# Kernel tuning notes

Measured on AMD Instinct MI355X. Metric: run time of the kernel, lower is better.

The kernel has to match this reference:

```python
import jax, jax.numpy as jnp
import numpy as np

COMMITMENT_COST = 0.25


def setup_inputs() -> dict:
    key = jax.random.key(0)
    k1, k2 = jax.random.split(key)
    n_embeddings, embedding_dim = 1024, 256
    x = jax.random.normal(k1, (32, 2048, embedding_dim), dtype=jnp.float32)
    r = 1.0 / n_embeddings
    embedding = jax.random.uniform(k2, (n_embeddings, embedding_dim),
                                   dtype=jnp.float32, minval=-r, maxval=r)
    return {"x": x, "embedding": embedding}


def reference(x, embedding):
    M, D = embedding.shape
    # x is detached before flattening in the original quantize()
    x_flat = jax.lax.stop_gradient(x).reshape(-1, D)  # [N, D]
    distances = (jnp.sum(embedding * embedding, axis=1)
                 + jnp.sum(x_flat * x_flat, axis=1, keepdims=True)
                 - 2.0 * (x_flat @ embedding.T))  # [N, M]
    indices = jnp.argmin(distances, axis=-1)  # [N] int
    quantized = embedding[indices].reshape(x.shape)  # gather + view_as(x)
    # commitment loss: quantized is detached in the loss term
    e_latent_loss = jnp.mean(jnp.square(x - jax.lax.stop_gradient(quantized)))
    loss = COMMITMENT_COST * e_latent_loss
    return quantized, loss, indices
```

## Files before the change

kernel.cpp:

```cpp
#include <hip/hip_runtime.h>

#define N_ROWS   65536
#define D        256
#define D4       64
#define M        1024
#define LOSS_OFF 16777216
#define IDX_OFF  16777217
#define COMMIT_SCALE (0.25f / 16777216.0f)
#define E_SCALE  1024.0f
#define C_SCALE  0.001953125f

typedef _Float16 f16x8 __attribute__((ext_vector_type(8)));
typedef _Float16 f16x4 __attribute__((ext_vector_type(4)));
typedef float    f32x4 __attribute__((ext_vector_type(4)));

__device__ __forceinline__ float np_block128(const float* __restrict__ a, int l) {
    float r0 = __fmul_rn(a[l +   0], a[l +   0]);
    float r1 = __fmul_rn(a[l +  16], a[l +  16]);
    float r2 = __fmul_rn(a[l +  32], a[l +  32]);
    float r3 = __fmul_rn(a[l +  48], a[l +  48]);
    float r4 = __fmul_rn(a[l +  64], a[l +  64]);
    float r5 = __fmul_rn(a[l +  80], a[l +  80]);
    float r6 = __fmul_rn(a[l +  96], a[l +  96]);
    float r7 = __fmul_rn(a[l + 112], a[l + 112]);
    return __fadd_rn(__fadd_rn(__fadd_rn(r0, r1), __fadd_rn(r2, r3)),
                     __fadd_rn(__fadd_rn(r4, r5), __fadd_rn(r6, r7)));
}
__device__ __forceinline__ float np_reduce16(float v) {
    float s = __fadd_rn(v, __shfl_down(v, 8));
    s = __fadd_rn(s, __shfl_down(s, 4));
    s = __fadd_rn(s, __shfl_down(s, 2));
    s = __fadd_rn(s, __shfl_down(s, 1));
    return s;
}

__global__ __launch_bounds__(256) void norms_kernel(
    const float4* __restrict__ x4, const float4* __restrict__ emb4,
    float* __restrict__ bsq, float* __restrict__ esq,
    _Float16* __restrict__ e_hi, _Float16* __restrict__ e_mid,
    float* __restrict__ loss_slot) {
    __shared__ float rowbuf[16 * 260];
    const int tid = threadIdx.x;
    const float4* src4;
    float* dst;
    int row0;
    const bool is_emb = blockIdx.x >= 4096;
    if (!is_emb) {
        row0 = blockIdx.x * 16;
        src4 = x4 + (size_t)row0 * 64;
        dst = bsq + row0;
    } else {
        row0 = (blockIdx.x - 4096) * 16;
        src4 = emb4 + (size_t)row0 * 64;
        dst = esq + row0;
    }
    #pragma unroll
    for (int p = 0; p < 4; ++p) {
        const int f = tid + p * 256;
        const int r = f >> 6, c4 = f & 63;
        *(float4*)&rowbuf[r * 260 + c4 * 4] = src4[f];
    }
    __syncthreads();
    const int l = tid & 15, g = tid >> 4;
    const float* base = &rowbuf[g * 260];
    const float v0 = np_block128(base, l);
    const float v1 = np_block128(base + 128, l);
    const float t0 = np_reduce16(v0);
    const float t1 = np_reduce16(v1);
    if (l == 0) dst[g] = __fadd_rn(t0, t1);
    if (blockIdx.x == 0 && tid == 0) *loss_slot = 0.0f;

    if (is_emb) {
        #pragma unroll
        for (int p = 0; p < 4; ++p) {
            const int f = tid + p * 256;
            const int r = f >> 6, k4 = f & 63;
            const int code = row0 + r;
            const int kc = k4 >> 3, k8 = k4 & 7;
            const int q = k8 >> 1, half = k8 & 1;
            const int jt = code >> 7, cl = code & 127;
            const int cg = cl >> 4, lmc = cl & 15;
            float4 v = *(const float4*)&rowbuf[r * 260 + k4 * 4];
            float a[4] = {v.x * E_SCALE, v.y * E_SCALE,
                          v.z * E_SCALE, v.w * E_SCALE};
            f16x4 hi, mid;
            #pragma unroll
            for (int j = 0; j < 4; ++j) {
                _Float16 h = (_Float16)a[j];
                float rr = __fsub_rn(a[j], (float)h);
                hi[j] = h;
                mid[j] = (_Float16)rr;
            }
            const size_t ofs = (size_t)kc * 32768 + (size_t)jt * 4096
                             + (size_t)(cg * 64 + q * 16 + lmc) * 8 + half * 4;
            *(f16x4*)&e_hi[ofs]  = hi;
            *(f16x4*)&e_mid[ofs] = mid;
        }
    }
}

__global__ __launch_bounds__(256, 2) void argmin_mfma_kernel(
    const float* __restrict__ x,
    const _Float16* __restrict__ e_hi, const _Float16* __restrict__ e_mid,
    const float* __restrict__ esq, const float* __restrict__ bsq,
    float* __restrict__ idx_out_f, int* __restrict__ idx_out_i) {
    __shared__ float esq_lds[1024];
    __shared__ float red_d[64][2];
    __shared__ int   red_i[64][2];

    const int tid = threadIdx.x;
    const int w = tid >> 6, lane = tid & 63;
    const int w_row = w >> 1, w_col = w & 1;
    const int lm = lane & 15, q = lane >> 4;
    const int row0 = blockIdx.x * 64;

    f16x8 a_hi[2][8], a_mid[2][8];
    #pragma unroll
    for (int fm = 0; fm < 2; ++fm) {
        const float* xr = x + (size_t)(row0 + w_row * 32 + fm * 16 + lm) * D + q * 8;
        #pragma unroll
        for (int kc = 0; kc < 8; ++kc) {
            float4 v0 = *(const float4*)(xr + kc * 32);
            float4 v1 = *(const float4*)(xr + kc * 32 + 4);
            float e[8] = {v0.x, v0.y, v0.z, v0.w, v1.x, v1.y, v1.z, v1.w};
            #pragma unroll
            for (int j = 0; j < 8; ++j) {
                _Float16 h = (_Float16)e[j];
                float r = __fsub_rn(e[j], (float)h);
                a_hi[fm][kc][j]  = h;
                a_mid[fm][kc][j] = (_Float16)r;
            }
        }
    }
    float bq[2][4];
    #pragma unroll
    for (int fm = 0; fm < 2; ++fm)
        #pragma unroll
        for (int r = 0; r < 4; ++r)
            bq[fm][r] = bsq[row0 + w_row * 32 + fm * 16 + q * 4 + r];

    *(float4*)&esq_lds[tid * 4] = ((const float4*)esq)[tid];
    __syncthreads();

    float best[2][4] = {{3.0e38f, 3.0e38f, 3.0e38f, 3.0e38f},
                        {3.0e38f, 3.0e38f, 3.0e38f, 3.0e38f}};
    int bidx[2][4] = {{0, 0, 0, 0}, {0, 0, 0, 0}};

    const int fofs = (w_col * 4) * 512 + lane * 8;
    for (int jt = 0; jt < 8; ++jt) {
        const int j0 = jt * 128;
        f32x4 acc[2][4] = {};
        #pragma unroll
        for (int kc = 0; kc < 8; ++kc) {
            const size_t cb = (size_t)kc * 32768 + (size_t)jt * 4096 + fofs;
            f16x8 bh[4], bm[4];
            #pragma unroll
            for (int fn = 0; fn < 4; ++fn) {
                bh[fn] = *(const f16x8*)&e_hi[cb + fn * 512];
                bm[fn] = *(const f16x8*)&e_mid[cb + fn * 512];
            }
            #pragma unroll
            for (int fm = 0; fm < 2; ++fm)
                #pragma unroll
                for (int fn = 0; fn < 4; ++fn) {
                    acc[fm][fn] = __builtin_amdgcn_mfma_f32_16x16x32_f16(
                        a_hi[fm][kc], bh[fn], acc[fm][fn], 0, 0, 0);
                    acc[fm][fn] = __builtin_amdgcn_mfma_f32_16x16x32_f16(
                        a_mid[fm][kc], bh[fn], acc[fm][fn], 0, 0, 0);
                    acc[fm][fn] = __builtin_amdgcn_mfma_f32_16x16x32_f16(
                        a_hi[fm][kc], bm[fn], acc[fm][fn], 0, 0, 0);
                }
        }
        #pragma unroll
        for (int fn = 0; fn < 4; ++fn) {
            const int j = j0 + w_col * 64 + fn * 16 + lm;
            const float eq = esq_lds[j];
            #pragma unroll
            for (int fm = 0; fm < 2; ++fm)
                #pragma unroll
                for (int r = 0; r < 4; ++r) {
                    const float d = __fsub_rn(__fadd_rn(eq, bq[fm][r]),
                                              acc[fm][fn][r] * C_SCALE);
                    if (d < best[fm][r]) { best[fm][r] = d; bidx[fm][r] = j; }
                }
        }
    }
    #pragma unroll
    for (int fm = 0; fm < 2; ++fm)
        #pragma unroll
        for (int r = 0; r < 4; ++r) {
            float d = best[fm][r]; int i = bidx[fm][r];
            #pragma unroll
            for (int mv = 1; mv <= 8; mv <<= 1) {
                const float d2 = __shfl_xor(d, mv, 64);
                const int   i2 = __shfl_xor(i, mv, 64);
                if (d2 < d || (d2 == d && i2 < i)) { d = d2; i = i2; }
            }
            best[fm][r] = d; bidx[fm][r] = i;
        }
    __syncthreads();
    if (lm == 0) {
        #pragma unroll
        for (int fm = 0; fm < 2; ++fm)
            #pragma unroll
            for (int r = 0; r < 4; ++r) {
                const int rl = w_row * 32 + fm * 16 + q * 4 + r;
                red_d[rl][w_col] = best[fm][r];
                red_i[rl][w_col] = bidx[fm][r];
            }
    }
    __syncthreads();
    if (tid < 64) {
        float d0 = red_d[tid][0]; int i0 = red_i[tid][0];
        const float d1 = red_d[tid][1]; const int i1 = red_i[tid][1];
        if (d1 < d0 || (d1 == d0 && i1 < i0)) { d0 = d1; i0 = i1; }
        idx_out_f[row0 + tid] = (float)i0;
        idx_out_i[row0 + tid] = i0;
    }
}

__global__ __launch_bounds__(256) void gather_loss_kernel(
    const float4* __restrict__ x4, const float4* __restrict__ emb4,
    const int* __restrict__ idx, float4* __restrict__ q4,
    float* __restrict__ loss_slot) {
    const int base = blockIdx.x * 256 + threadIdx.x;
    float acc = 0.0f;
    #pragma unroll
    for (int i = 0; i < 16; ++i) {
        const int f   = base + i * (1024 * 256);
        const int row = f >> 6;
        const int c4  = f & 63;
        const int e   = idx[row];
        float4 qv = emb4[e * D4 + c4];
        float4 xv = x4[f];
        q4[f] = qv;
        const float dx = xv.x - qv.x, dy = xv.y - qv.y;
        const float dz = xv.z - qv.z, dw = xv.w - qv.w;
        acc += dx * dx + dy * dy + dz * dz + dw * dw;
    }
    #pragma unroll
    for (int off = 32; off; off >>= 1) acc += __shfl_down(acc, off, 64);
    __shared__ float wsum[4];
    const int lane = threadIdx.x & 63, w = threadIdx.x >> 6;
    if (lane == 0) wsum[w] = acc;
    __syncthreads();
    if (threadIdx.x == 0) {
        atomicAdd(loss_slot, (wsum[0] + wsum[1] + wsum[2] + wsum[3]) * COMMIT_SCALE);
    }
}

extern "C" void kernel_launch(void* const* d_in, const int* in_sizes, int n_in,
                              void* d_out, int out_size, void* d_ws, size_t ws_size,
                              hipStream_t stream) {
    const float* x   = (const float*)d_in[0];
    const float* emb = (const float*)d_in[1];
    float* out = (float*)d_out;
    float*    bsq  = (float*)d_ws;
    float*    esq  = bsq + N_ROWS;
    int*      idx  = (int*)(esq + M);
    _Float16* e_hi = (_Float16*)(idx + N_ROWS);
    _Float16* e_mid = e_hi + (size_t)M * D;

    norms_kernel<<<4096 + M / 16, 256, 0, stream>>>((const float4*)x,
                                                    (const float4*)emb,
                                                    bsq, esq, e_hi, e_mid,
                                                    out + LOSS_OFF);
    argmin_mfma_kernel<<<N_ROWS / 64, 256, 0, stream>>>(x, e_hi, e_mid,
                                                        esq, bsq,
                                                        out + IDX_OFF, idx);
    gather_loss_kernel<<<1024, 256, 0, stream>>>((const float4*)x,
                                                 (const float4*)emb, idx,
                                                 (float4*)out, out + LOSS_OFF);
}
```

Baseline: 267.7 us.

## Double-buffer codebook fragments via async global-to-LDS DMA per wave

Codebook hi/mid fp16 fragments were loaded directly from global memory into registers before each MFMA group. They now arrive through per-wave double-buffered LDS slots filled with global_load_lds async copies, issued two chunks ahead and guarded by vmcnt waits. Wave priority is raised around the MFMA block so math overlaps the next DMA. This aims to hide global load latency, at the cost of 64KB of extra LDS per block, which may reduce occupancy below the launch-bound target of 2 blocks.

```diff
diff --git a/kernel.cpp b/kernel.cpp
--- a/kernel.cpp
+++ b/kernel.cpp
@@ -13,6 +13,12 @@
 typedef _Float16 f16x8 __attribute__((ext_vector_type(8)));
 typedef _Float16 f16x4 __attribute__((ext_vector_type(4)));
 typedef float    f32x4 __attribute__((ext_vector_type(4)));
+
+__device__ __forceinline__ void async_copy16(const void* g, void* l) {
+    __builtin_amdgcn_global_load_lds(
+        (const __attribute__((address_space(1))) unsigned int*)g,
+        (__attribute__((address_space(3))) unsigned int*)l, 16, 0, 0);
+}
 
 __device__ __forceinline__ float np_block128(const float* __restrict__ a, int l) {
     float r0 = __fmul_rn(a[l +   0], a[l +   0]);
@@ -104,6 +110,7 @@
     const _Float16* __restrict__ e_hi, const _Float16* __restrict__ e_mid,
     const float* __restrict__ esq, const float* __restrict__ bsq,
     float* __restrict__ idx_out_f, int* __restrict__ idx_out_i) {
+    __shared__ __attribute__((aligned(16))) _Float16 buf[4][2][4096];
     __shared__ float esq_lds[1024];
     __shared__ float red_d[64][2];
     __shared__ int   red_i[64][2];
@@ -114,6 +121,26 @@
     const int lm = lane & 15, q = lane >> 4;
     const int row0 = blockIdx.x * 64;
 
+    auto dma = [&](int c, int s) {
+        const int jt = c >> 3, kc = c & 7;
+        const size_t gofs = (size_t)kc * 65536 + (size_t)jt * 8192
+                          + (size_t)w_col * 4096 + (size_t)lane * 16;
+        const char* gh = (const char*)e_hi + gofs;
+        const char* gm = (const char*)e_mid + gofs;
+        _Float16* lh  = &buf[w][s][0];
+        _Float16* lmm = &buf[w][s][2048];
+        async_copy16(gh,        lh);
+        async_copy16(gh + 1024, lh + 512);
+        async_copy16(gh + 2048, lh + 1024);
+        async_copy16(gh + 3072, lh + 1536);
+        async_copy16(gm,        lmm);
+        async_copy16(gm + 1024, lmm + 512);
+        async_copy16(gm + 2048, lmm + 1024);
+        async_copy16(gm + 3072, lmm + 1536);
+    };
+
+    dma(0, 0);
+
     f16x8 a_hi[2][8], a_mid[2][8];
     #pragma unroll
     for (int fm = 0; fm < 2; ++fm) {
@@ -140,25 +167,32 @@
             bq[fm][r] = bsq[row0 + w_row * 32 + fm * 16 + q * 4 + r];
 
     *(float4*)&esq_lds[tid * 4] = ((const float4*)esq)[tid];
-    __syncthreads();
+
+    asm volatile("s_waitcnt vmcnt(0) lgkmcnt(0)" ::: "memory");
+    __syncthreads();
+    dma(1, 1);
 
     float best[2][4] = {{3.0e38f, 3.0e38f, 3.0e38f, 3.0e38f},
                         {3.0e38f, 3.0e38f, 3.0e38f, 3.0e38f}};
     int bidx[2][4] = {{0, 0, 0, 0}, {0, 0, 0, 0}};
 
-    const int fofs = (w_col * 4) * 512 + lane * 8;
     for (int jt = 0; jt < 8; ++jt) {
         const int j0 = jt * 128;
         f32x4 acc[2][4] = {};
         #pragma unroll
         for (int kc = 0; kc < 8; ++kc) {
-            const size_t cb = (size_t)kc * 32768 + (size_t)jt * 4096 + fofs;
+            const int c = jt * 8 + kc;
+            const int P = c & 1;
             f16x8 bh[4], bm[4];
             #pragma unroll
             for (int fn = 0; fn < 4; ++fn) {
-                bh[fn] = *(const f16x8*)&e_hi[cb + fn * 512];
-                bm[fn] = *(const f16x8*)&e_mid[cb + fn * 512];
-            }
+                bh[fn] = *(const f16x8*)&buf[w][P][fn * 512 + lane * 8];
+                bm[fn] = *(const f16x8*)&buf[w][P][2048 + fn * 512 + lane * 8];
+            }
+            asm volatile("s_waitcnt lgkmcnt(0)" ::: "memory");
+            __builtin_amdgcn_sched_barrier(0);
+            if (c < 62) dma(c + 2, P);
+            __builtin_amdgcn_s_setprio(1);
             #pragma unroll
             for (int fm = 0; fm < 2; ++fm)
                 #pragma unroll
@@ -170,6 +204,12 @@
                     acc[fm][fn] = __builtin_amdgcn_mfma_f32_16x16x32_f16(
                         a_hi[fm][kc], bm[fn], acc[fm][fn], 0, 0, 0);
                 }
+            __builtin_amdgcn_s_setprio(0);
+            if (c < 62)
+                asm volatile("s_waitcnt vmcnt(8)" ::: "memory");
+            else if (c == 62)
+                asm volatile("s_waitcnt vmcnt(0)" ::: "memory");
+            __builtin_amdgcn_sched_barrier(0);
         }
         #pragma unroll
         for (int fn = 0; fn < 4; ++fn) {
```

New measurement: 244.9 us. 1.09x faster.

## Stage codebook tiles through double-buffered LDS via async global_load_lds

Applied to the files above, without the earlier changes.

Codebook hi/mid fp16 tiles were read straight from global memory into registers by every wave. They are now copied cooperatively into a double-buffered 64KB shared-memory staging area with global_load_lds, and the next group is prefetched while the current one feeds the MFMAs. Each wave loads its B fragments from LDS and raises its scheduling priority around the MFMA block. The aim is to hide global load latency and remove duplicate codebook reads across waves. The costs are a barrier per group, a larger LDS footprint that may limit occupancy to two blocks per CU, and full vmcnt waits that serialize part of the pipeline.

```diff
diff --git a/kernel.cpp b/kernel.cpp
--- a/kernel.cpp
+++ b/kernel.cpp
@@ -13,6 +13,12 @@
 typedef _Float16 f16x8 __attribute__((ext_vector_type(8)));
 typedef _Float16 f16x4 __attribute__((ext_vector_type(4)));
 typedef float    f32x4 __attribute__((ext_vector_type(4)));
+
+__device__ __forceinline__ void async_copy16(const void* g, void* l) {
+    __builtin_amdgcn_global_load_lds(
+        (const __attribute__((address_space(1))) unsigned int*)g,
+        (__attribute__((address_space(3))) unsigned int*)l, 16, 0, 0);
+}
 
 __device__ __forceinline__ float np_block128(const float* __restrict__ a, int l) {
     float r0 = __fmul_rn(a[l +   0], a[l +   0]);
@@ -104,6 +110,7 @@
     const _Float16* __restrict__ e_hi, const _Float16* __restrict__ e_mid,
     const float* __restrict__ esq, const float* __restrict__ bsq,
     float* __restrict__ idx_out_f, int* __restrict__ idx_out_i) {
+    __shared__ __attribute__((aligned(16))) _Float16 buf[2][16384];
     __shared__ float esq_lds[1024];
     __shared__ float red_d[64][2];
     __shared__ int   red_i[64][2];
@@ -114,6 +121,21 @@
     const int lm = lane & 15, q = lane >> 4;
     const int row0 = blockIdx.x * 64;
 
+    const int p_sub = w >> 1, p_plane = w & 1;
+    const _Float16* p_src = p_plane ? e_mid : e_hi;
+    auto dma_group = [&](int g, int s) {
+        const int jt = g >> 2, kc0 = (g & 3) * 2;
+        const char* gp = (const char*)p_src
+                       + (size_t)(kc0 + p_sub) * 65536 + (size_t)jt * 8192
+                       + (size_t)lane * 16;
+        _Float16* lp = &buf[s][p_sub * 8192 + p_plane * 4096];
+        #pragma unroll
+        for (int u = 0; u < 8; ++u)
+            async_copy16(gp + u * 1024, lp + u * 512);
+    };
+
+    dma_group(0, 0);
+
     f16x8 a_hi[2][8], a_mid[2][8];
     #pragma unroll
     for (int fm = 0; fm < 2; ++fm) {
@@ -140,36 +162,53 @@
             bq[fm][r] = bsq[row0 + w_row * 32 + fm * 16 + q * 4 + r];
 
     *(float4*)&esq_lds[tid * 4] = ((const float4*)esq)[tid];
+
+    asm volatile("s_waitcnt vmcnt(0) lgkmcnt(0)" ::: "memory");
     __syncthreads();
 
     float best[2][4] = {{3.0e38f, 3.0e38f, 3.0e38f, 3.0e38f},
                         {3.0e38f, 3.0e38f, 3.0e38f, 3.0e38f}};
     int bidx[2][4] = {{0, 0, 0, 0}, {0, 0, 0, 0}};
 
-    const int fofs = (w_col * 4) * 512 + lane * 8;
     for (int jt = 0; jt < 8; ++jt) {
         const int j0 = jt * 128;
         f32x4 acc[2][4] = {};
         #pragma unroll
-        for (int kc = 0; kc < 8; ++kc) {
-            const size_t cb = (size_t)kc * 32768 + (size_t)jt * 4096 + fofs;
-            f16x8 bh[4], bm[4];
-            #pragma unroll
-            for (int fn = 0; fn < 4; ++fn) {
-                bh[fn] = *(const f16x8*)&e_hi[cb + fn * 512];
-                bm[fn] = *(const f16x8*)&e_mid[cb + fn * 512];
-            }
-            #pragma unroll
-            for (int fm = 0; fm < 2; ++fm)
+        for (int gi = 0; gi < 4; ++gi) {
+            const int g = jt * 4 + gi;
+            if (g) {
+                asm volatile("s_waitcnt vmcnt(0) lgkmcnt(0)\n\t"
+                             "s_barrier" ::: "memory");
+                __builtin_amdgcn_sched_barrier(0);
+            }
+            if (g < 31) dma_group(g + 1, (g + 1) & 1);
+            const int s = g & 1;
+            #pragma unroll
+            for (int sub = 0; sub < 2; ++sub) {
+                const int kc = gi * 2 + sub;
+                f16x8 bh[4], bm[4];
+                const int fb = sub * 8192 + (w_col * 4) * 512 + lane * 8;
                 #pragma unroll
                 for (int fn = 0; fn < 4; ++fn) {
-                    acc[fm][fn] = __builtin_amdgcn_mfma_f32_16x16x32_f16(
-                        a_hi[fm][kc], bh[fn], acc[fm][fn], 0, 0, 0);
-                    acc[fm][fn] = __builtin_amdgcn_mfma_f32_16x16x32_f16(
-                        a_mid[fm][kc], bh[fn], acc[fm][fn], 0, 0, 0);
-                    acc[fm][fn] = __builtin_amdgcn_mfma_f32_16x16x32_f16(
-                        a_hi[fm][kc], bm[fn], acc[fm][fn], 0, 0, 0);
+                    bh[fn] = *(const f16x8*)&buf[s][fb + fn * 512];
+                    bm[fn] = *(const f16x8*)&buf[s][fb + 4096 + fn * 512];
                 }
+                asm volatile("s_waitcnt lgkmcnt(0)" ::: "memory");
+                __builtin_amdgcn_sched_barrier(0);
+                __builtin_amdgcn_s_setprio(1);
+                #pragma unroll
+                for (int fm = 0; fm < 2; ++fm)
+                    #pragma unroll
+                    for (int fn = 0; fn < 4; ++fn) {
+                        acc[fm][fn] = __builtin_amdgcn_mfma_f32_16x16x32_f16(
+                            a_hi[fm][kc], bh[fn], acc[fm][fn], 0, 0, 0);
+                        acc[fm][fn] = __builtin_amdgcn_mfma_f32_16x16x32_f16(
+                            a_mid[fm][kc], bh[fn], acc[fm][fn], 0, 0, 0);
+                        acc[fm][fn] = __builtin_amdgcn_mfma_f32_16x16x32_f16(
+                            a_hi[fm][kc], bm[fn], acc[fm][fn], 0, 0, 0);
+                    }
+                __builtin_amdgcn_s_setprio(0);
+            }
         }
         #pragma unroll
         for (int fn = 0; fn < 4; ++fn) {
```

After: 234.1 us. -12.6%, faster.
